# Kernel tuning notes

Measured on AMD Instinct MI355X. Metric: run time of the kernel, lower is better.

The kernel has to match this reference:

```python
import jax, jax.numpy as jnp
import numpy as np
from jax import lax

B = 16384  # batch; original torch module runs unbatched (1,5,27), we vectorize over B


def _conv(x, w, b, ph):
    # NCHW conv with kernel (kh,1), padding (ph,0), stride 1
    y = lax.conv_general_dilated(x, w, (1, 1), [(ph, ph), (0, 0)],
                                 dimension_numbers=('NCHW', 'OIHW', 'NCHW'))
    return y + b[None, :, None, None]


def _sl(x, w, b):
    # Semi_Linear: shared Linear applied over every (channel, height) slice ->
    # algebraically a single batched matmul on the last axis. w: (out,in)
    return jnp.einsum('bchw,ow->bcho', x, w) + b


def setup_inputs() -> dict:
    key = jax.random.key(0)
    ks = iter(jax.random.split(key, 40))
    def p(shape):
        return jax.random.normal(next(ks), shape, jnp.float32) * 0.05
    d = dict(
        x=jax.random.normal(next(ks), (B, 1, 5, 27), jnp.float32),
        w0a=p((5, 1, 3, 1)), b0a=p((5,)),
        wl0=p((18, 27)), bl0=p((18,)),
        w0b=p((25, 5, 3, 1)), b0b=p((25,)),
        w0c=p((25, 1, 1, 1)), b0c=p((25,)),
        wr0=p((18, 27)), br0=p((18,)),
        w1=p((75, 25, 2, 1)), b1=p((75,)),
        wl1=p((10, 18)), bl1=p((10,)),
        w2=p((125, 75, 2, 1)), b2=p((125,)),
        wa=p((125, 25, 3, 1)), ba=p((125,)),
        wra=p((10, 18)), bra=p((10,)),
        w0=p((300, 125, 2, 1)), b0=p((300,)),
        wl2=p((5, 10)), bl2=p((5,)),
        w0b2=p((512, 300, 2, 1)), b0b2=p((512,)),
        w0c2=p((512, 125, 3, 1)), b0c2=p((512,)),
        wr02=p((5, 10)), br02=p((5,)),
    )
    return d


def reference(x, w0a, b0a, wl0, bl0, w0b, b0b, w0c, b0c, wr0, br0,
              w1, b1, wl1, bl1, w2, b2, wa, ba, wra, bra,
              w0, b0, wl2, bl2, w0b2, b0b2, w0c2, b0c2, wr02, br02):
    # stage 0
    z = _conv(x, w0a, b0a, 1)                      # (B,5,5,27)
    z = jax.nn.relu(_sl(z, wl0, bl0))              # (B,5,5,18)
    z = _conv(z, w0b, b0b, 1)                      # (B,25,5,18)
    y = _conv(_sl(x, wr0, br0), w0c, b0c, 0)       # (B,25,5,18)
    x1 = z + y
    # stage 1
    z = _conv(x1, w1, b1, 0)                       # (B,75,4,18)
    z = jax.nn.relu(_sl(z, wl1, bl1))              # (B,75,4,10)
    z = _conv(z, w2, b2, 0)                        # (B,125,3,10)
    y = _conv(_sl(x1, wra, bra), wa, ba, 0)        # (B,125,3,10)
    x2 = z + y
    # stage 2
    z = _conv(x2, w0, b0, 0)                       # (B,300,2,10)
    z = jax.nn.relu(_sl(z, wl2, bl2))              # (B,300,2,5)
    z = _conv(z, w0b2, b0b2, 0)                    # (B,512,1,5)
    y = _conv(_sl(x2, wr02, br02), w0c2, b0c2, 0)  # (B,512,1,5)
    return z + y
```

## Files before the change

### kernel.cpp

```cpp
#include <hip/hip_runtime.h>
#include <stdint.h>


#define WB2T_OFF 0
#define WC2T_OFF 307200
#define W0T_OFF  499200
#define W1T_OFF  574200
#define WAT_OFF  577950
#define W2T_OFF  587325
#define SUM0_OFF 606075
#define SUM1_OFF 606093
#define SUM2_OFF 606103
#define WT_TOTAL 606108

__global__ __launch_bounds__(256)
void transpose_w(const float* __restrict__ w1, const float* __restrict__ wa,
                 const float* __restrict__ w2, const float* __restrict__ w0,
                 const float* __restrict__ wb2, const float* __restrict__ wc2,
                 const float* __restrict__ wl0, const float* __restrict__ wl1,
                 const float* __restrict__ wl2,
                 float* __restrict__ ws) {
  int i = blockIdx.x * 256 + threadIdx.x;
  if (i < 3750) {
    int co = i / 50, k = i % 50;
    ws[W1T_OFF + k*75 + co] = w1[i];
  } else if (i < 13125) {
    int j = i - 3750; int co = j / 75, k = j % 75;
    ws[WAT_OFF + k*125 + co] = wa[j];
  } else if (i < 31875) {
    int j = i - 13125; int co = j / 150, k = j % 150;
    ws[W2T_OFF + k*125 + co] = w2[j];
  } else if (i < 106875) {
    int j = i - 31875; int co = j / 250, k = j % 250;
    ws[W0T_OFF + k*300 + co] = w0[j];
  } else if (i < 414075) {
    int j = i - 106875; int co = j / 600, k = j % 600;
    ws[WB2T_OFF + k*512 + co] = wb2[j];
  } else if (i < 606075) {
    int j = i - 414075; int co = j / 375, k = j % 375;
    ws[WC2T_OFF + k*512 + co] = wc2[j];
  } else if (i < 606093) {
    int j = i - 606075; float s = 0.f;
    for (int w = 0; w < 27; ++w) s += wl0[j*27 + w];
    ws[SUM0_OFF + j] = s;
  } else if (i < 606103) {
    int j = i - 606093; float s = 0.f;
    for (int w = 0; w < 18; ++w) s += wl1[j*18 + w];
    ws[SUM1_OFF + j] = s;
  } else if (i < 606108) {
    int j = i - 606103; float s = 0.f;
    for (int w = 0; w < 10; ++w) s += wl2[j*10 + w];
    ws[SUM2_OFF + j] = s;
  }
}

template<int N>
__device__ __forceinline__ void ldrow(float* r, const float* p) {
  #pragma unroll
  for (int i = 0; i < N/4; ++i) {
    float4 q = reinterpret_cast<const float4*>(p)[i];
    r[4*i+0] = q.x; r[4*i+1] = q.y; r[4*i+2] = q.z; r[4*i+3] = q.w;
  }
}
template<int N>
__device__ __forceinline__ void strow(float* p, const float* r) {
  #pragma unroll
  for (int i = 0; i < N/4; ++i) {
    float4 q; q.x = r[4*i+0]; q.y = r[4*i+1]; q.z = r[4*i+2]; q.w = r[4*i+3];
    reinterpret_cast<float4*>(p)[i] = q;
  }
}

#define POOL   10112
#define X1_O   0
#define SX_O   2500
#define XS0_O  2640
#define T90_O  2740
#define Z0SL_O 2840
#define X1S_O  2500
#define Z1S_O  4500
#define T2_O   8100
#define X2_O   0
#define T3_O   8100
#define X2S_O  4500
#define Z2S_O  0

__global__ __launch_bounds__(256, 2)
void fused_net(const float* __restrict__ xg,
  const float* __restrict__ w0a_, const float* __restrict__ b0a_,
  const float* __restrict__ wl0_, const float* __restrict__ bl0_,
  const float* __restrict__ w0b_, const float* __restrict__ b0b_,
  const float* __restrict__ w0c_, const float* __restrict__ b0c_,
  const float* __restrict__ wr0_, const float* __restrict__ br0_,
  const float* __restrict__ b1_,
  const float* __restrict__ wl1_, const float* __restrict__ bl1_,
  const float* __restrict__ b2_,
  const float* __restrict__ ba_,
  const float* __restrict__ wra_, const float* __restrict__ bra_,
  const float* __restrict__ b0_,
  const float* __restrict__ wl2_, const float* __restrict__ bl2_,
  const float* __restrict__ b0b2_,
  const float* __restrict__ b0c2_,
  const float* __restrict__ wr02_,const float* __restrict__ br02_,
  const float* __restrict__ w1t, const float* __restrict__ wat,
  const float* __restrict__ w2t, const float* __restrict__ w0t,
  const float* __restrict__ wb2t, const float* __restrict__ wc2t,
  const float* __restrict__ sums,
  float* __restrict__ outg, int Btot)
{
  __shared__ __align__(16) float S[2*POOL];
  const int tid = threadIdx.x;
  const int b0 = blockIdx.x * 2;

  for (int i = tid; i < 270; i += 256) {
    int samp = i / 135, j = i % 135;
    int h = j / 27, w = j % 27;
    float v = 0.f;
    if (b0 + samp < Btot) v = xg[(size_t)(b0 + samp) * 135 + j];
    S[samp*POOL + SX_O + h*28 + w] = v;
  }
  __syncthreads();

  if (tid < 30) {
    int samp = tid / 15, r = tid % 15, h = r / 3, o0 = (r % 3) * 6;
    float* P = S + samp*POOL;
    float row[28]; ldrow<28>(row, P + SX_O + h*28);
    float xs[6], t9[6];
    #pragma unroll
    for (int k = 0; k < 6; ++k) { xs[k] = 0.f; t9[k] = br0_[o0 + k]; }
    for (int w = 0; w < 27; ++w) {
      float rv = row[w];
      #pragma unroll
      for (int k = 0; k < 6; ++k) {
        xs[k] += rv * wl0_[(o0 + k)*27 + w];
        t9[k] += rv * wr0_[(o0 + k)*27 + w];
      }
    }
    #pragma unroll
    for (int k = 0; k < 6; ++k) {
      P[XS0_O + h*20 + o0 + k] = xs[k];
      P[T90_O + h*20 + o0 + k] = t9[k];
    }
  }
  __syncthreads();

  if (tid < 50) {
    int samp = tid / 25, r = tid % 25, co = r / 5, h = r % 5;
    float* P = S + samp*POOL;
    float acc[20];
    float bc = b0a_[co];
    #pragma unroll
    for (int o = 0; o < 18; ++o) acc[o] = bc * sums[o] + bl0_[o];
    acc[18] = 0.f; acc[19] = 0.f;
    #pragma unroll
    for (int dh = 0; dh < 3; ++dh) {
      int hi = h + dh - 1;
      if (hi >= 0 && hi < 5) {
        float wf = w0a_[co*3 + dh];
        float row[20]; ldrow<20>(row, P + XS0_O + hi*20);
        #pragma unroll
        for (int o = 0; o < 18; ++o) acc[o] += row[o] * wf;
      }
    }
    #pragma unroll
    for (int o = 0; o < 18; ++o) acc[o] = fmaxf(acc[o], 0.f);
    strow<20>(P + Z0SL_O + (co*5 + h)*20, acc);
  }
  __syncthreads();

  if (tid < 250) {
    int samp = tid / 125, r = tid % 125, h = r / 25, co = r % 25;
    float* P = S + samp*POOL;
    float tr[20]; ldrow<20>(tr, P + T90_O + h*20);
    float wc = w0c_[co];
    float base = b0b_[co] + b0c_[co];
    float acc[20];
    #pragma unroll
    for (int o = 0; o < 18; ++o) acc[o] = base + tr[o]*wc;
    acc[18] = 0.f; acc[19] = 0.f;
    #pragma unroll
    for (int dh = 0; dh < 3; ++dh) {
      int hi = h + dh - 1;
      if (hi >= 0 && hi < 5) {
        #pragma unroll
        for (int ci = 0; ci < 5; ++ci) {
          float wgt = w0b_[(co*5 + ci)*3 + dh];
          float row[20]; ldrow<20>(row, P + Z0SL_O + (ci*5 + hi)*20);
          #pragma unroll
          for (int o = 0; o < 18; ++o) acc[o] += row[o] * wgt;
        }
      }
    }
    strow<20>(P + X1_O + (co*5 + h)*20, acc);
  }
  __syncthreads();

  if (tid < 250) {
    int samp = tid / 125, r = tid % 125, h = r / 25, c = r % 25;
    float* P = S + samp*POOL;
    float row[20]; ldrow<20>(row, P + X1_O + (c*5 + h)*20);
    float t2[12], x1s[12];
    #pragma unroll
    for (int o = 0; o < 10; ++o) {
      float a = bra_[o], s = 0.f;
      #pragma unroll
      for (int w = 0; w < 18; ++w) {
        a += row[w] * wra_[o*18 + w];
        s += row[w] * wl1_[o*18 + w];
      }
      t2[o] = a; x1s[o] = s;
    }
    t2[10] = t2[11] = 0.f; x1s[10] = x1s[11] = 0.f;
    strow<12>(P + T2_O  + (c*5 + h)*12, t2);
    strow<12>(P + X1S_O + (c*5 + h)*12, x1s);
  }
  __syncthreads();

  for (int t = tid; t < 300; t += 256) {
    int samp = t / 150, r = t % 150, co = r >> 1, h0 = (r & 1) * 2;
    float* P = S + samp*POOL;
    float acc[2][10];
    float bc = b1_[co];
    #pragma unroll
    for (int o = 0; o < 10; ++o) {
      float b = bc * sums[18 + o] + bl1_[o];
      acc[0][o] = b; acc[1][o] = b;
    }
    for (int ci = 0; ci < 25; ++ci) {
      float wx = w1t[(ci*2 + 0)*75 + co];
      float wy = w1t[(ci*2 + 1)*75 + co];
      float r0[12], r1[12], r2[12];
      ldrow<12>(r0, P + X1S_O + (ci*5 + h0    )*12);
      ldrow<12>(r1, P + X1S_O + (ci*5 + h0 + 1)*12);
      ldrow<12>(r2, P + X1S_O + (ci*5 + h0 + 2)*12);
      #pragma unroll
      for (int o = 0; o < 10; ++o) {
        acc[0][o] += r0[o]*wx + r1[o]*wy;
        acc[1][o] += r1[o]*wx + r2[o]*wy;
      }
    }
    #pragma unroll
    for (int hh = 0; hh < 2; ++hh) {
      float out[12];
      #pragma unroll
      for (int o = 0; o < 10; ++o) out[o] = fmaxf(acc[hh][o], 0.f);
      out[10] = 0.f; out[11] = 0.f;
      strow<12>(P + Z1S_O + (co*4 + h0 + hh)*12, out);
    }
  }
  __syncthreads();

  if (tid < 250) {
    int samp = tid / 125, co = tid % 125;
    float* P = S + samp*POOL;
    float acc[3][10];
    float bias = b2_[co] + ba_[co];
    #pragma unroll
    for (int h = 0; h < 3; ++h)
      #pragma unroll
      for (int w = 0; w < 10; ++w) acc[h][w] = bias;
    for (int ci = 0; ci < 25; ++ci) {
      float wf0 = wat[(ci*3 + 0)*125 + co];
      float wf1 = wat[(ci*3 + 1)*125 + co];
      float wf2 = wat[(ci*3 + 2)*125 + co];
      float rr[5][12];
      #pragma unroll
      for (int hh = 0; hh < 5; ++hh) ldrow<12>(rr[hh], P + T2_O + (ci*5 + hh)*12);
      #pragma unroll
      for (int h = 0; h < 3; ++h)
        #pragma unroll
        for (int w = 0; w < 10; ++w)
          acc[h][w] += rr[h][w]*wf0 + rr[h+1][w]*wf1 + rr[h+2][w]*wf2;
    }
    for (int ci = 0; ci < 75; ++ci) {
      float wx = w2t[(ci*2 + 0)*125 + co];
      float wy = w2t[(ci*2 + 1)*125 + co];
      float rr[4][12];
      #pragma unroll
      for (int hh = 0; hh < 4; ++hh) ldrow<12>(rr[hh], P + Z1S_O + (ci*4 + hh)*12);
      #pragma unroll
      for (int h = 0; h < 3; ++h)
        #pragma unroll
        for (int w = 0; w < 10; ++w)
          acc[h][w] += rr[h][w]*wx + rr[h+1][w]*wy;
    }
    #pragma unroll
    for (int h = 0; h < 3; ++h) {
      float out[12];
      #pragma unroll
      for (int w = 0; w < 10; ++w) out[w] = acc[h][w];
      out[10] = 0.f; out[11] = 0.f;
      strow<12>(P + X2_O + (co*3 + h)*12, out);
    }
  }
  __syncthreads();

  if (tid < 250) {
    int samp = tid / 125, c = tid % 125;
    float* P = S + samp*POOL;
    float rr[3][12];
    #pragma unroll
    for (int h = 0; h < 3; ++h) ldrow<12>(rr[h], P + X2_O + (c*3 + h)*12);
    float t3[16];
    #pragma unroll
    for (int h = 0; h < 3; ++h) {
      float x2s[8];
      #pragma unroll
      for (int o = 0; o < 5; ++o) {
        float a = br02_[o], s = 0.f;
        #pragma unroll
        for (int w = 0; w < 10; ++w) {
          a += rr[h][w] * wr02_[o*10 + w];
          s += rr[h][w] * wl2_[o*10 + w];
        }
        t3[h*5 + o] = a; x2s[o] = s;
      }
      x2s[5] = x2s[6] = x2s[7] = 0.f;
      strow<8>(P + X2S_O + (c*3 + h)*8, x2s);
    }
    t3[15] = 0.f;
    strow<16>(P + T3_O + c*16, t3);
  }
  __syncthreads();

  for (int t = tid; t < 300; t += 256) {
    int samp = t / 150, q2 = t % 150, co = q2 * 2;
    float* P = S + samp*POOL;
    float acc[2][2][5];
    #pragma unroll
    for (int j = 0; j < 2; ++j) {
      float bc = b0_[co + j];
      #pragma unroll
      for (int o = 0; o < 5; ++o) {
        float b = bc * sums[28 + o] + bl2_[o];
        acc[j][0][o] = b; acc[j][1][o] = b;
      }
    }
    for (int ci = 0; ci < 125; ++ci) {
      float2 wxv = *reinterpret_cast<const float2*>(w0t + (ci*2 + 0)*300 + co);
      float2 wyv = *reinterpret_cast<const float2*>(w0t + (ci*2 + 1)*300 + co);
      float a0[8], a1[8], a2[8];
      ldrow<8>(a0, P + X2S_O + (ci*3 + 0)*8);
      ldrow<8>(a1, P + X2S_O + (ci*3 + 1)*8);
      ldrow<8>(a2, P + X2S_O + (ci*3 + 2)*8);
      float wx[2] = {wxv.x, wxv.y};
      float wy[2] = {wyv.x, wyv.y};
      #pragma unroll
      for (int j = 0; j < 2; ++j)
        #pragma unroll
        for (int o = 0; o < 5; ++o) {
          acc[j][0][o] += a0[o]*wx[j] + a1[o]*wy[j];
          acc[j][1][o] += a1[o]*wx[j] + a2[o]*wy[j];
        }
    }
    #pragma unroll
    for (int j = 0; j < 2; ++j) {
      float out[12];
      #pragma unroll
      for (int h = 0; h < 2; ++h)
        #pragma unroll
        for (int o = 0; o < 5; ++o) out[h*5 + o] = fmaxf(acc[j][h][o], 0.f);
      out[10] = 0.f; out[11] = 0.f;
      strow<12>(P + Z2S_O + (co + j)*12, out);
    }
  }
  __syncthreads();

  {
    int samp = tid >> 7, coq = tid & 127;
    int co = coq * 4;
    float* P = S + samp*POOL;
    float acc[4][5];
    #pragma unroll
    for (int j = 0; j < 4; ++j) {
      float bb = b0b2_[co + j] + b0c2_[co + j];
      #pragma unroll
      for (int w = 0; w < 5; ++w) acc[j][w] = bb;
    }
    for (int ci = 0; ci < 300; ++ci) {
      float a[12]; ldrow<12>(a, P + Z2S_O + ci*12);
      float4 uxv = *reinterpret_cast<const float4*>(wb2t + (ci*2 + 0)*512 + co);
      float4 uyv = *reinterpret_cast<const float4*>(wb2t + (ci*2 + 1)*512 + co);
      float ux[4] = {uxv.x, uxv.y, uxv.z, uxv.w};
      float uy[4] = {uyv.x, uyv.y, uyv.z, uyv.w};
      #pragma unroll
      for (int j = 0; j < 4; ++j)
        #pragma unroll
        for (int w = 0; w < 5; ++w)
          acc[j][w] += a[w]*ux[j] + a[5 + w]*uy[j];
    }
    for (int ci = 0; ci < 125; ++ci) {
      float t3[16]; ldrow<16>(t3, P + T3_O + ci*16);
      float4 u0v = *reinterpret_cast<const float4*>(wc2t + (ci*3 + 0)*512 + co);
      float4 u1v = *reinterpret_cast<const float4*>(wc2t + (ci*3 + 1)*512 + co);
      float4 u2v = *reinterpret_cast<const float4*>(wc2t + (ci*3 + 2)*512 + co);
      float u0[4] = {u0v.x, u0v.y, u0v.z, u0v.w};
      float u1[4] = {u1v.x, u1v.y, u1v.z, u1v.w};
      float u2[4] = {u2v.x, u2v.y, u2v.z, u2v.w};
      #pragma unroll
      for (int j = 0; j < 4; ++j)
        #pragma unroll
        for (int w = 0; w < 5; ++w)
          acc[j][w] += t3[w]*u0[j] + t3[5 + w]*u1[j] + t3[10 + w]*u2[j];
    }
    if (b0 + samp < Btot) {
      float* ob = outg + (size_t)(b0 + samp) * 2560 + co*5;
      float flat[20];
      #pragma unroll
      for (int j = 0; j < 4; ++j)
        #pragma unroll
        for (int w = 0; w < 5; ++w) flat[j*5 + w] = acc[j][w];
      strow<20>(ob, flat);
    }
  }
}

extern "C" void kernel_launch(void* const* d_in, const int* in_sizes, int n_in,
                              void* d_out, int out_size, void* d_ws, size_t ws_size,
                              hipStream_t stream) {
  (void)in_sizes; (void)n_in; (void)ws_size;
  const float* p[31];
  for (int i = 0; i < 31; ++i) p[i] = (const float*)d_in[i];
  float* ws = (float*)d_ws;

  transpose_w<<<(WT_TOTAL + 255) / 256, 256, 0, stream>>>(
      p[11] , p[17] , p[15] , p[21] ,
      p[25] , p[27] ,
      p[3] , p[13] , p[23] , ws);

  int Btot = out_size / 2560;
  if (Btot <= 0) return;
  int nb = (Btot + 1) >> 1;
  fused_net<<<nb, 256, 0, stream>>>(
      p[0],
      p[1],  p[2],  p[3],  p[4],  p[5],  p[6],  p[7],  p[8],  p[9],  p[10],
      p[12],
      p[13], p[14],
      p[16],
      p[18],
      p[19], p[20],
      p[22],
      p[23], p[24],
      p[26],
      p[28],
      p[29], p[30],
      ws + W1T_OFF, ws + WAT_OFF, ws + W2T_OFF, ws + W0T_OFF,
      ws + WB2T_OFF, ws + WC2T_OFF,
      ws + SUM0_OFF,
      (float*)d_out, Btot);
}
```

Before: 3.075 ms.

## Concentrate late stages on two wavefronts with more output channels per thread

The stage-1 second conv, stage-2 first conv and final 512-channel conv now run on only 128 of the 256 threads, one wavefront per sample. Each thread computes 2, 5 or 8 output channels instead of 1, 2 or 4. A block-parity rotation picks which half of the block is active, so odd and even blocks use different SIMD slots. The goal is more register-level reuse of shared-memory activation rows and wider weight loads per FMA. The cost is half the threads sitting idle in these stages, higher register pressure, and possible occupancy loss.

After: 4.020 ms. 30.7% more time.

```diff
diff --git a/kernel.cpp b/kernel.cpp
--- a/kernel.cpp
+++ b/kernel.cpp
@@ -111,6 +111,7 @@
   __shared__ __align__(16) float S[2*POOL];
   const int tid = threadIdx.x;
   const int b0 = blockIdx.x * 2;
+  const int rot = ((int)(blockIdx.x & 1)) << 7;
 
   for (int i = tid; i < 270; i += 256) {
     int samp = i / 135, j = i % 135;
@@ -250,47 +251,75 @@
   }
   __syncthreads();
 
-  if (tid < 250) {
-    int samp = tid / 125, co = tid % 125;
-    float* P = S + samp*POOL;
-    float acc[3][10];
-    float bias = b2_[co] + ba_[co];
-    #pragma unroll
-    for (int h = 0; h < 3; ++h)
-      #pragma unroll
-      for (int w = 0; w < 10; ++w) acc[h][w] = bias;
-    for (int ci = 0; ci < 25; ++ci) {
-      float wf0 = wat[(ci*3 + 0)*125 + co];
-      float wf1 = wat[(ci*3 + 1)*125 + co];
-      float wf2 = wat[(ci*3 + 2)*125 + co];
-      float rr[5][12];
-      #pragma unroll
-      for (int hh = 0; hh < 5; ++hh) ldrow<12>(rr[hh], P + T2_O + (ci*5 + hh)*12);
-      #pragma unroll
-      for (int h = 0; h < 3; ++h)
-        #pragma unroll
-        for (int w = 0; w < 10; ++w)
-          acc[h][w] += rr[h][w]*wf0 + rr[h+1][w]*wf1 + rr[h+2][w]*wf2;
-    }
-    for (int ci = 0; ci < 75; ++ci) {
-      float wx = w2t[(ci*2 + 0)*125 + co];
-      float wy = w2t[(ci*2 + 1)*125 + co];
-      float rr[4][12];
-      #pragma unroll
-      for (int hh = 0; hh < 4; ++hh) ldrow<12>(rr[hh], P + Z1S_O + (ci*4 + hh)*12);
-      #pragma unroll
-      for (int h = 0; h < 3; ++h)
-        #pragma unroll
-        for (int w = 0; w < 10; ++w)
-          acc[h][w] += rr[h][w]*wx + rr[h+1][w]*wy;
-    }
-    #pragma unroll
-    for (int h = 0; h < 3; ++h) {
-      float out[12];
-      #pragma unroll
-      for (int w = 0; w < 10; ++w) out[w] = acc[h][w];
-      out[10] = 0.f; out[11] = 0.f;
-      strow<12>(P + X2_O + (co*3 + h)*12, out);
+  {
+    int at = tid - rot;
+    if (at >= 0 && at < 128) {
+      int samp = at >> 6, lane = at & 63;
+      if (lane < 63) {
+        int co0 = lane * 2;
+        int two = (co0 + 1 < 125);
+        int co1 = two ? co0 + 1 : co0;
+        float* P = S + samp*POOL;
+        float acc[2][3][10];
+        float bi0 = b2_[co0] + ba_[co0];
+        float bi1 = b2_[co1] + ba_[co1];
+        #pragma unroll
+        for (int h = 0; h < 3; ++h)
+          #pragma unroll
+          for (int w = 0; w < 10; ++w) { acc[0][h][w] = bi0; acc[1][h][w] = bi1; }
+        for (int ci = 0; ci < 25; ++ci) {
+          float wf[2][3];
+          #pragma unroll
+          for (int d = 0; d < 3; ++d) {
+            wf[0][d] = wat[(ci*3 + d)*125 + co0];
+            wf[1][d] = wat[(ci*3 + d)*125 + co1];
+          }
+          float rr[5][12];
+          #pragma unroll
+          for (int hh = 0; hh < 5; ++hh) ldrow<12>(rr[hh], P + T2_O + (ci*5 + hh)*12);
+          #pragma unroll
+          for (int j = 0; j < 2; ++j)
+            #pragma unroll
+            for (int h = 0; h < 3; ++h)
+              #pragma unroll
+              for (int w = 0; w < 10; ++w)
+                acc[j][h][w] += rr[h][w]*wf[j][0] + rr[h+1][w]*wf[j][1] + rr[h+2][w]*wf[j][2];
+        }
+        for (int ci = 0; ci < 75; ++ci) {
+          float wx0 = w2t[(ci*2 + 0)*125 + co0];
+          float wx1 = w2t[(ci*2 + 0)*125 + co1];
+          float wy0 = w2t[(ci*2 + 1)*125 + co0];
+          float wy1 = w2t[(ci*2 + 1)*125 + co1];
+          float rr[4][12];
+          #pragma unroll
+          for (int hh = 0; hh < 4; ++hh) ldrow<12>(rr[hh], P + Z1S_O + (ci*4 + hh)*12);
+          #pragma unroll
+          for (int h = 0; h < 3; ++h)
+            #pragma unroll
+            for (int w = 0; w < 10; ++w) {
+              acc[0][h][w] += rr[h][w]*wx0 + rr[h+1][w]*wy0;
+              acc[1][h][w] += rr[h][w]*wx1 + rr[h+1][w]*wy1;
+            }
+        }
+        #pragma unroll
+        for (int h = 0; h < 3; ++h) {
+          float out[12];
+          #pragma unroll
+          for (int w = 0; w < 10; ++w) out[w] = acc[0][h][w];
+          out[10] = 0.f; out[11] = 0.f;
+          strow<12>(P + X2_O + (co0*3 + h)*12, out);
+        }
+        if (two) {
+          #pragma unroll
+          for (int h = 0; h < 3; ++h) {
+            float out[12];
+            #pragma unroll
+            for (int w = 0; w < 10; ++w) out[w] = acc[1][h][w];
+            out[10] = 0.f; out[11] = 0.f;
+            strow<12>(P + X2_O + (co1*3 + h)*12, out);
+          }
+        }
+      }
     }
   }
   __syncthreads();
@@ -323,94 +352,102 @@
   }
   __syncthreads();
 
-  for (int t = tid; t < 300; t += 256) {
-    int samp = t / 150, q2 = t % 150, co = q2 * 2;
-    float* P = S + samp*POOL;
-    float acc[2][2][5];
-    #pragma unroll
-    for (int j = 0; j < 2; ++j) {
-      float bc = b0_[co + j];
-      #pragma unroll
-      for (int o = 0; o < 5; ++o) {
-        float b = bc * sums[28 + o] + bl2_[o];
-        acc[j][0][o] = b; acc[j][1][o] = b;
-      }
-    }
-    for (int ci = 0; ci < 125; ++ci) {
-      float2 wxv = *reinterpret_cast<const float2*>(w0t + (ci*2 + 0)*300 + co);
-      float2 wyv = *reinterpret_cast<const float2*>(w0t + (ci*2 + 1)*300 + co);
-      float a0[8], a1[8], a2[8];
-      ldrow<8>(a0, P + X2S_O + (ci*3 + 0)*8);
-      ldrow<8>(a1, P + X2S_O + (ci*3 + 1)*8);
-      ldrow<8>(a2, P + X2S_O + (ci*3 + 2)*8);
-      float wx[2] = {wxv.x, wxv.y};
-      float wy[2] = {wyv.x, wyv.y};
-      #pragma unroll
-      for (int j = 0; j < 2; ++j)
-        #pragma unroll
-        for (int o = 0; o < 5; ++o) {
-          acc[j][0][o] += a0[o]*wx[j] + a1[o]*wy[j];
-          acc[j][1][o] += a1[o]*wx[j] + a2[o]*wy[j];
-        }
-    }
-    #pragma unroll
-    for (int j = 0; j < 2; ++j) {
-      float out[12];
-      #pragma unroll
-      for (int h = 0; h < 2; ++h)
-        #pragma unroll
-        for (int o = 0; o < 5; ++o) out[h*5 + o] = fmaxf(acc[j][h][o], 0.f);
-      out[10] = 0.f; out[11] = 0.f;
-      strow<12>(P + Z2S_O + (co + j)*12, out);
-    }
-  }
-  __syncthreads();
-
   {
-    int samp = tid >> 7, coq = tid & 127;
-    int co = coq * 4;
-    float* P = S + samp*POOL;
-    float acc[4][5];
-    #pragma unroll
-    for (int j = 0; j < 4; ++j) {
-      float bb = b0b2_[co + j] + b0c2_[co + j];
-      #pragma unroll
-      for (int w = 0; w < 5; ++w) acc[j][w] = bb;
-    }
-    for (int ci = 0; ci < 300; ++ci) {
-      float a[12]; ldrow<12>(a, P + Z2S_O + ci*12);
-      float4 uxv = *reinterpret_cast<const float4*>(wb2t + (ci*2 + 0)*512 + co);
-      float4 uyv = *reinterpret_cast<const float4*>(wb2t + (ci*2 + 1)*512 + co);
-      float ux[4] = {uxv.x, uxv.y, uxv.z, uxv.w};
-      float uy[4] = {uyv.x, uyv.y, uyv.z, uyv.w};
-      #pragma unroll
-      for (int j = 0; j < 4; ++j)
-        #pragma unroll
-        for (int w = 0; w < 5; ++w)
-          acc[j][w] += a[w]*ux[j] + a[5 + w]*uy[j];
-    }
-    for (int ci = 0; ci < 125; ++ci) {
-      float t3[16]; ldrow<16>(t3, P + T3_O + ci*16);
-      float4 u0v = *reinterpret_cast<const float4*>(wc2t + (ci*3 + 0)*512 + co);
-      float4 u1v = *reinterpret_cast<const float4*>(wc2t + (ci*3 + 1)*512 + co);
-      float4 u2v = *reinterpret_cast<const float4*>(wc2t + (ci*3 + 2)*512 + co);
-      float u0[4] = {u0v.x, u0v.y, u0v.z, u0v.w};
-      float u1[4] = {u1v.x, u1v.y, u1v.z, u1v.w};
-      float u2[4] = {u2v.x, u2v.y, u2v.z, u2v.w};
-      #pragma unroll
-      for (int j = 0; j < 4; ++j)
-        #pragma unroll
-        for (int w = 0; w < 5; ++w)
-          acc[j][w] += t3[w]*u0[j] + t3[5 + w]*u1[j] + t3[10 + w]*u2[j];
-    }
-    if (b0 + samp < Btot) {
-      float* ob = outg + (size_t)(b0 + samp) * 2560 + co*5;
-      float flat[20];
-      #pragma unroll
-      for (int j = 0; j < 4; ++j)
-        #pragma unroll
-        for (int w = 0; w < 5; ++w) flat[j*5 + w] = acc[j][w];
-      strow<20>(ob, flat);
+    int at = tid - rot;
+    if (at >= 0 && at < 128) {
+      int samp = at >> 6, lane = at & 63;
+      if (lane < 60) {
+        int co = lane * 5;
+        float* P = S + samp*POOL;
+        float acc[5][2][5];
+        #pragma unroll
+        for (int j = 0; j < 5; ++j) {
+          float bc = b0_[co + j];
+          #pragma unroll
+          for (int o = 0; o < 5; ++o) {
+            float b = bc * sums[28 + o] + bl2_[o];
+            acc[j][0][o] = b; acc[j][1][o] = b;
+          }
+        }
+        for (int ci = 0; ci < 125; ++ci) {
+          float wx[5], wy[5];
+          #pragma unroll
+          for (int j = 0; j < 5; ++j) {
+            wx[j] = w0t[(ci*2 + 0)*300 + co + j];
+            wy[j] = w0t[(ci*2 + 1)*300 + co + j];
+          }
+          float a0[8], a1[8], a2[8];
+          ldrow<8>(a0, P + X2S_O + (ci*3 + 0)*8);
+          ldrow<8>(a1, P + X2S_O + (ci*3 + 1)*8);
+          ldrow<8>(a2, P + X2S_O + (ci*3 + 2)*8);
+          #pragma unroll
+          for (int j = 0; j < 5; ++j)
+            #pragma unroll
+            for (int o = 0; o < 5; ++o) {
+              acc[j][0][o] += a0[o]*wx[j] + a1[o]*wy[j];
+              acc[j][1][o] += a1[o]*wx[j] + a2[o]*wy[j];
+            }
+        }
+        #pragma unroll
+        for (int j = 0; j < 5; ++j) {
+          float out[12];
+          #pragma unroll
+          for (int h = 0; h < 2; ++h)
+            #pragma unroll
+            for (int o = 0; o < 5; ++o) out[h*5 + o] = fmaxf(acc[j][h][o], 0.f);
+          out[10] = 0.f; out[11] = 0.f;
+          strow<12>(P + Z2S_O + (co + j)*12, out);
+        }
+      }
+    }
+  }
+  __syncthreads();
+
+  {
+    int at = tid - rot;
+    if (at >= 0 && at < 128) {
+      int samp = at >> 6, lane = at & 63;
+      int co = lane * 8;
+      float* P = S + samp*POOL;
+      float acc[8][5];
+      #pragma unroll
+      for (int j = 0; j < 8; ++j) {
+        float bb = b0b2_[co + j] + b0c2_[co + j];
+        #pragma unroll
+        for (int w = 0; w < 5; ++w) acc[j][w] = bb;
+      }
+      for (int ci = 0; ci < 300; ++ci) {
+        float a[12]; ldrow<12>(a, P + Z2S_O + ci*12);
+        float ux[8], uy[8];
+        ldrow<8>(ux, wb2t + (ci*2 + 0)*512 + co);
+        ldrow<8>(uy, wb2t + (ci*2 + 1)*512 + co);
+        #pragma unroll
+        for (int j = 0; j < 8; ++j)
+          #pragma unroll
+          for (int w = 0; w < 5; ++w)
+            acc[j][w] += a[w]*ux[j] + a[5 + w]*uy[j];
+      }
+      for (int ci = 0; ci < 125; ++ci) {
+        float t3[16]; ldrow<16>(t3, P + T3_O + ci*16);
+        float u0[8], u1[8], u2[8];
+        ldrow<8>(u0, wc2t + (ci*3 + 0)*512 + co);
+        ldrow<8>(u1, wc2t + (ci*3 + 1)*512 + co);
+        ldrow<8>(u2, wc2t + (ci*3 + 2)*512 + co);
+        #pragma unroll
+        for (int j = 0; j < 8; ++j)
+          #pragma unroll
+          for (int w = 0; w < 5; ++w)
+            acc[j][w] += t3[w]*u0[j] + t3[5 + w]*u1[j] + t3[10 + w]*u2[j];
+      }
+      if (b0 + samp < Btot) {
+        float* ob = outg + (size_t)(b0 + samp) * 2560 + co*5;
+        float flat[40];
+        #pragma unroll
+        for (int j = 0; j < 8; ++j)
+          #pragma unroll
+          for (int w = 0; w < 5; ++w) flat[j*5 + w] = acc[j][w];
+        strow<40>(ob, flat);
+      }
     }
   }
 }
```

## Move later-stage intermediates to global scratch and use persistent grid-stride blocks

Applied to the files above, without the earlier changes.

Shrinks shared memory per block to the stage-0 buffers and moves stage 1 and stage 2 intermediates into per-block global workspace scratch. The kernel becomes persistent: at most 1024 blocks (fewer if workspace is small) loop over sample pairs. The aim is higher occupancy from less LDS per block, at the cost of routing the heavy later-stage reads through global memory and cache instead of LDS. There is also a risk of too few blocks if the workspace is small.

Result: slower. 5.905 ms (+92.0%).

```diff
diff --git a/kernel.cpp b/kernel.cpp
--- a/kernel.cpp
+++ b/kernel.cpp
@@ -71,19 +71,21 @@
   }
 }
 
-#define POOL   10112
-#define X1_O   0
+#define LPOOL  3340
+#define X1L_O  0
 #define SX_O   2500
 #define XS0_O  2640
 #define T90_O  2740
 #define Z0SL_O 2840
+
+#define GPOOL  10112
+#define X2_O   0
+#define Z2S_O  0
 #define X1S_O  2500
 #define Z1S_O  4500
+#define X2S_O  4500
 #define T2_O   8100
-#define X2_O   0
 #define T3_O   8100
-#define X2S_O  4500
-#define Z2S_O  0
 
 __global__ __launch_bounds__(256, 2)
 void fused_net(const float* __restrict__ xg,
@@ -106,319 +108,326 @@
   const float* __restrict__ w2t, const float* __restrict__ w0t,
   const float* __restrict__ wb2t, const float* __restrict__ wc2t,
   const float* __restrict__ sums,
-  float* __restrict__ outg, int Btot)
+  float* scr,
+  float* __restrict__ outg, int Btot, int npairs, int NB)
 {
-  __shared__ __align__(16) float S[2*POOL];
+  __shared__ __align__(16) float S[2*LPOOL];
   const int tid = threadIdx.x;
-  const int b0 = blockIdx.x * 2;
-
-  for (int i = tid; i < 270; i += 256) {
-    int samp = i / 135, j = i % 135;
-    int h = j / 27, w = j % 27;
-    float v = 0.f;
-    if (b0 + samp < Btot) v = xg[(size_t)(b0 + samp) * 135 + j];
-    S[samp*POOL + SX_O + h*28 + w] = v;
-  }
-  __syncthreads();
-
-  if (tid < 30) {
-    int samp = tid / 15, r = tid % 15, h = r / 3, o0 = (r % 3) * 6;
-    float* P = S + samp*POOL;
-    float row[28]; ldrow<28>(row, P + SX_O + h*28);
-    float xs[6], t9[6];
-    #pragma unroll
-    for (int k = 0; k < 6; ++k) { xs[k] = 0.f; t9[k] = br0_[o0 + k]; }
-    for (int w = 0; w < 27; ++w) {
-      float rv = row[w];
+  float* G = scr + (size_t)blockIdx.x * (2*GPOOL);
+
+  for (int p = blockIdx.x; p < npairs; p += NB) {
+    const int b0 = p * 2;
+
+    for (int i = tid; i < 270; i += 256) {
+      int samp = i / 135, j = i % 135;
+      int h = j / 27, w = j % 27;
+      float v = 0.f;
+      if (b0 + samp < Btot) v = xg[(size_t)(b0 + samp) * 135 + j];
+      S[samp*LPOOL + SX_O + h*28 + w] = v;
+    }
+    __syncthreads();
+
+    if (tid < 30) {
+      int samp = tid / 15, r = tid % 15, h = r / 3, o0 = (r % 3) * 6;
+      float* L = S + samp*LPOOL;
+      float row[28]; ldrow<28>(row, L + SX_O + h*28);
+      float xs[6], t9[6];
+      #pragma unroll
+      for (int k = 0; k < 6; ++k) { xs[k] = 0.f; t9[k] = br0_[o0 + k]; }
+      for (int w = 0; w < 27; ++w) {
+        float rv = row[w];
+        #pragma unroll
+        for (int k = 0; k < 6; ++k) {
+          xs[k] += rv * wl0_[(o0 + k)*27 + w];
+          t9[k] += rv * wr0_[(o0 + k)*27 + w];
+        }
+      }
       #pragma unroll
       for (int k = 0; k < 6; ++k) {
-        xs[k] += rv * wl0_[(o0 + k)*27 + w];
-        t9[k] += rv * wr0_[(o0 + k)*27 + w];
-      }
-    }
-    #pragma unroll
-    for (int k = 0; k < 6; ++k) {
-      P[XS0_O + h*20 + o0 + k] = xs[k];
-      P[T90_O + h*20 + o0 + k] = t9[k];
-    }
-  }
-  __syncthreads();
-
-  if (tid < 50) {
-    int samp = tid / 25, r = tid % 25, co = r / 5, h = r % 5;
-    float* P = S + samp*POOL;
-    float acc[20];
-    float bc = b0a_[co];
-    #pragma unroll
-    for (int o = 0; o < 18; ++o) acc[o] = bc * sums[o] + bl0_[o];
-    acc[18] = 0.f; acc[19] = 0.f;
-    #pragma unroll
-    for (int dh = 0; dh < 3; ++dh) {
-      int hi = h + dh - 1;
-      if (hi >= 0 && hi < 5) {
-        float wf = w0a_[co*3 + dh];
-        float row[20]; ldrow<20>(row, P + XS0_O + hi*20);
-        #pragma unroll
-        for (int o = 0; o < 18; ++o) acc[o] += row[o] * wf;
-      }
-    }
-    #pragma unroll
-    for (int o = 0; o < 18; ++o) acc[o] = fmaxf(acc[o], 0.f);
-    strow<20>(P + Z0SL_O + (co*5 + h)*20, acc);
-  }
-  __syncthreads();
-
-  if (tid < 250) {
-    int samp = tid / 125, r = tid % 125, h = r / 25, co = r % 25;
-    float* P = S + samp*POOL;
-    float tr[20]; ldrow<20>(tr, P + T90_O + h*20);
-    float wc = w0c_[co];
-    float base = b0b_[co] + b0c_[co];
-    float acc[20];
-    #pragma unroll
-    for (int o = 0; o < 18; ++o) acc[o] = base + tr[o]*wc;
-    acc[18] = 0.f; acc[19] = 0.f;
-    #pragma unroll
-    for (int dh = 0; dh < 3; ++dh) {
-      int hi = h + dh - 1;
-      if (hi >= 0 && hi < 5) {
-        #pragma unroll
-        for (int ci = 0; ci < 5; ++ci) {
-          float wgt = w0b_[(co*5 + ci)*3 + dh];
-          float row[20]; ldrow<20>(row, P + Z0SL_O + (ci*5 + hi)*20);
-          #pragma unroll
-          for (int o = 0; o < 18; ++o) acc[o] += row[o] * wgt;
-        }
-      }
-    }
-    strow<20>(P + X1_O + (co*5 + h)*20, acc);
-  }
-  __syncthreads();
-
-  if (tid < 250) {
-    int samp = tid / 125, r = tid % 125, h = r / 25, c = r % 25;
-    float* P = S + samp*POOL;
-    float row[20]; ldrow<20>(row, P + X1_O + (c*5 + h)*20);
-    float t2[12], x1s[12];
-    #pragma unroll
-    for (int o = 0; o < 10; ++o) {
-      float a = bra_[o], s = 0.f;
-      #pragma unroll
-      for (int w = 0; w < 18; ++w) {
-        a += row[w] * wra_[o*18 + w];
-        s += row[w] * wl1_[o*18 + w];
-      }
-      t2[o] = a; x1s[o] = s;
-    }
-    t2[10] = t2[11] = 0.f; x1s[10] = x1s[11] = 0.f;
-    strow<12>(P + T2_O  + (c*5 + h)*12, t2);
-    strow<12>(P + X1S_O + (c*5 + h)*12, x1s);
-  }
-  __syncthreads();
-
-  for (int t = tid; t < 300; t += 256) {
-    int samp = t / 150, r = t % 150, co = r >> 1, h0 = (r & 1) * 2;
-    float* P = S + samp*POOL;
-    float acc[2][10];
-    float bc = b1_[co];
-    #pragma unroll
-    for (int o = 0; o < 10; ++o) {
-      float b = bc * sums[18 + o] + bl1_[o];
-      acc[0][o] = b; acc[1][o] = b;
-    }
-    for (int ci = 0; ci < 25; ++ci) {
-      float wx = w1t[(ci*2 + 0)*75 + co];
-      float wy = w1t[(ci*2 + 1)*75 + co];
-      float r0[12], r1[12], r2[12];
-      ldrow<12>(r0, P + X1S_O + (ci*5 + h0    )*12);
-      ldrow<12>(r1, P + X1S_O + (ci*5 + h0 + 1)*12);
-      ldrow<12>(r2, P + X1S_O + (ci*5 + h0 + 2)*12);
+        L[XS0_O + h*20 + o0 + k] = xs[k];
+        L[T90_O + h*20 + o0 + k] = t9[k];
+      }
+    }
+    __syncthreads();
+
+    if (tid < 50) {
+      int samp = tid / 25, r = tid % 25, co = r / 5, h = r % 5;
+      float* L = S + samp*LPOOL;
+      float acc[20];
+      float bc = b0a_[co];
+      #pragma unroll
+      for (int o = 0; o < 18; ++o) acc[o] = bc * sums[o] + bl0_[o];
+      acc[18] = 0.f; acc[19] = 0.f;
+      #pragma unroll
+      for (int dh = 0; dh < 3; ++dh) {
+        int hi = h + dh - 1;
+        if (hi >= 0 && hi < 5) {
+          float wf = w0a_[co*3 + dh];
+          float row[20]; ldrow<20>(row, L + XS0_O + hi*20);
+          #pragma unroll
+          for (int o = 0; o < 18; ++o) acc[o] += row[o] * wf;
+        }
+      }
+      #pragma unroll
+      for (int o = 0; o < 18; ++o) acc[o] = fmaxf(acc[o], 0.f);
+      strow<20>(L + Z0SL_O + (co*5 + h)*20, acc);
+    }
+    __syncthreads();
+
+    if (tid < 250) {
+      int samp = tid / 125, r = tid % 125, h = r / 25, co = r % 25;
+      float* L = S + samp*LPOOL;
+      float tr[20]; ldrow<20>(tr, L + T90_O + h*20);
+      float wc = w0c_[co];
+      float base = b0b_[co] + b0c_[co];
+      float acc[20];
+      #pragma unroll
+      for (int o = 0; o < 18; ++o) acc[o] = base + tr[o]*wc;
+      acc[18] = 0.f; acc[19] = 0.f;
+      #pragma unroll
+      for (int dh = 0; dh < 3; ++dh) {
+        int hi = h + dh - 1;
+        if (hi >= 0 && hi < 5) {
+          #pragma unroll
+          for (int ci = 0; ci < 5; ++ci) {
+            float wgt = w0b_[(co*5 + ci)*3 + dh];
+            float row[20]; ldrow<20>(row, L + Z0SL_O + (ci*5 + hi)*20);
+            #pragma unroll
+            for (int o = 0; o < 18; ++o) acc[o] += row[o] * wgt;
+          }
+        }
+      }
+      strow<20>(L + X1L_O + (co*5 + h)*20, acc);
+    }
+    __syncthreads();
+
+    if (tid < 250) {
+      int samp = tid / 125, r = tid % 125, h = r / 25, c = r % 25;
+      float* L = S + samp*LPOOL;
+      float* Gp = G + samp*GPOOL;
+      float row[20]; ldrow<20>(row, L + X1L_O + (c*5 + h)*20);
+      float t2[12], x1s[12];
       #pragma unroll
       for (int o = 0; o < 10; ++o) {
-        acc[0][o] += r0[o]*wx + r1[o]*wy;
-        acc[1][o] += r1[o]*wx + r2[o]*wy;
-      }
-    }
-    #pragma unroll
-    for (int hh = 0; hh < 2; ++hh) {
-      float out[12];
-      #pragma unroll
-      for (int o = 0; o < 10; ++o) out[o] = fmaxf(acc[hh][o], 0.f);
-      out[10] = 0.f; out[11] = 0.f;
-      strow<12>(P + Z1S_O + (co*4 + h0 + hh)*12, out);
-    }
-  }
-  __syncthreads();
-
-  if (tid < 250) {
-    int samp = tid / 125, co = tid % 125;
-    float* P = S + samp*POOL;
-    float acc[3][10];
-    float bias = b2_[co] + ba_[co];
-    #pragma unroll
-    for (int h = 0; h < 3; ++h)
-      #pragma unroll
-      for (int w = 0; w < 10; ++w) acc[h][w] = bias;
-    for (int ci = 0; ci < 25; ++ci) {
-      float wf0 = wat[(ci*3 + 0)*125 + co];
-      float wf1 = wat[(ci*3 + 1)*125 + co];
-      float wf2 = wat[(ci*3 + 2)*125 + co];
-      float rr[5][12];
-      #pragma unroll
-      for (int hh = 0; hh < 5; ++hh) ldrow<12>(rr[hh], P + T2_O + (ci*5 + hh)*12);
+        float a = bra_[o], s = 0.f;
+        #pragma unroll
+        for (int w = 0; w < 18; ++w) {
+          a += row[w] * wra_[o*18 + w];
+          s += row[w] * wl1_[o*18 + w];
+        }
+        t2[o] = a; x1s[o] = s;
+      }
+      t2[10] = t2[11] = 0.f; x1s[10] = x1s[11] = 0.f;
+      strow<12>(Gp + T2_O  + (c*5 + h)*12, t2);
+      strow<12>(Gp + X1S_O + (c*5 + h)*12, x1s);
+    }
+    __syncthreads();
+
+    for (int t = tid; t < 300; t += 256) {
+      int samp = t / 150, r = t % 150, co = r >> 1, h0 = (r & 1) * 2;
+      float* Gp = G + samp*GPOOL;
+      float acc[2][10];
+      float bc = b1_[co];
+      #pragma unroll
+      for (int o = 0; o < 10; ++o) {
+        float b = bc * sums[18 + o] + bl1_[o];
+        acc[0][o] = b; acc[1][o] = b;
+      }
+      for (int ci = 0; ci < 25; ++ci) {
+        float wx = w1t[(ci*2 + 0)*75 + co];
+        float wy = w1t[(ci*2 + 1)*75 + co];
+        float r0[12], r1[12], r2[12];
+        ldrow<12>(r0, Gp + X1S_O + (ci*5 + h0    )*12);
+        ldrow<12>(r1, Gp + X1S_O + (ci*5 + h0 + 1)*12);
+        ldrow<12>(r2, Gp + X1S_O + (ci*5 + h0 + 2)*12);
+        #pragma unroll
+        for (int o = 0; o < 10; ++o) {
+          acc[0][o] += r0[o]*wx + r1[o]*wy;
+          acc[1][o] += r1[o]*wx + r2[o]*wy;
+        }
+      }
+      #pragma unroll
+      for (int hh = 0; hh < 2; ++hh) {
+        float out[12];
+        #pragma unroll
+        for (int o = 0; o < 10; ++o) out[o] = fmaxf(acc[hh][o], 0.f);
+        out[10] = 0.f; out[11] = 0.f;
+        strow<12>(Gp + Z1S_O + (co*4 + h0 + hh)*12, out);
+      }
+    }
+    __syncthreads();
+
+    if (tid < 250) {
+      int samp = tid / 125, co = tid % 125;
+      float* Gp = G + samp*GPOOL;
+      float acc[3][10];
+      float bias = b2_[co] + ba_[co];
       #pragma unroll
       for (int h = 0; h < 3; ++h)
         #pragma unroll
-        for (int w = 0; w < 10; ++w)
-          acc[h][w] += rr[h][w]*wf0 + rr[h+1][w]*wf1 + rr[h+2][w]*wf2;
-    }
-    for (int ci = 0; ci < 75; ++ci) {
-      float wx = w2t[(ci*2 + 0)*125 + co];
-      float wy = w2t[(ci*2 + 1)*125 + co];
-      float rr[4][12];
-      #pragma unroll
-      for (int hh = 0; hh < 4; ++hh) ldrow<12>(rr[hh], P + Z1S_O + (ci*4 + hh)*12);
-      #pragma unroll
-      for (int h = 0; h < 3; ++h)
-        #pragma unroll
-        for (int w = 0; w < 10; ++w)
-          acc[h][w] += rr[h][w]*wx + rr[h+1][w]*wy;
-    }
-    #pragma unroll
-    for (int h = 0; h < 3; ++h) {
-      float out[12];
-      #pragma unroll
-      for (int w = 0; w < 10; ++w) out[w] = acc[h][w];
-      out[10] = 0.f; out[11] = 0.f;
-      strow<12>(P + X2_O + (co*3 + h)*12, out);
-    }
-  }
-  __syncthreads();
-
-  if (tid < 250) {
-    int samp = tid / 125, c = tid % 125;
-    float* P = S + samp*POOL;
-    float rr[3][12];
-    #pragma unroll
-    for (int h = 0; h < 3; ++h) ldrow<12>(rr[h], P + X2_O + (c*3 + h)*12);
-    float t3[16];
-    #pragma unroll
-    for (int h = 0; h < 3; ++h) {
-      float x2s[8];
-      #pragma unroll
-      for (int o = 0; o < 5; ++o) {
-        float a = br02_[o], s = 0.f;
-        #pragma unroll
-        for (int w = 0; w < 10; ++w) {
-          a += rr[h][w] * wr02_[o*10 + w];
-          s += rr[h][w] * wl2_[o*10 + w];
-        }
-        t3[h*5 + o] = a; x2s[o] = s;
-      }
-      x2s[5] = x2s[6] = x2s[7] = 0.f;
-      strow<8>(P + X2S_O + (c*3 + h)*8, x2s);
-    }
-    t3[15] = 0.f;
-    strow<16>(P + T3_O + c*16, t3);
-  }
-  __syncthreads();
-
-  for (int t = tid; t < 300; t += 256) {
-    int samp = t / 150, q2 = t % 150, co = q2 * 2;
-    float* P = S + samp*POOL;
-    float acc[2][2][5];
-    #pragma unroll
-    for (int j = 0; j < 2; ++j) {
-      float bc = b0_[co + j];
-      #pragma unroll
-      for (int o = 0; o < 5; ++o) {
-        float b = bc * sums[28 + o] + bl2_[o];
-        acc[j][0][o] = b; acc[j][1][o] = b;
-      }
-    }
-    for (int ci = 0; ci < 125; ++ci) {
-      float2 wxv = *reinterpret_cast<const float2*>(w0t + (ci*2 + 0)*300 + co);
-      float2 wyv = *reinterpret_cast<const float2*>(w0t + (ci*2 + 1)*300 + co);
-      float a0[8], a1[8], a2[8];
-      ldrow<8>(a0, P + X2S_O + (ci*3 + 0)*8);
-      ldrow<8>(a1, P + X2S_O + (ci*3 + 1)*8);
-      ldrow<8>(a2, P + X2S_O + (ci*3 + 2)*8);
-      float wx[2] = {wxv.x, wxv.y};
-      float wy[2] = {wyv.x, wyv.y};
-      #pragma unroll
-      for (int j = 0; j < 2; ++j)
+        for (int w = 0; w < 10; ++w) acc[h][w] = bias;
+      for (int ci = 0; ci < 25; ++ci) {
+        float wf0 = wat[(ci*3 + 0)*125 + co];
+        float wf1 = wat[(ci*3 + 1)*125 + co];
+        float wf2 = wat[(ci*3 + 2)*125 + co];
+        float rr[5][12];
+        #pragma unroll
+        for (int hh = 0; hh < 5; ++hh) ldrow<12>(rr[hh], Gp + T2_O + (ci*5 + hh)*12);
+        #pragma unroll
+        for (int h = 0; h < 3; ++h)
+          #pragma unroll
+          for (int w = 0; w < 10; ++w)
+            acc[h][w] += rr[h][w]*wf0 + rr[h+1][w]*wf1 + rr[h+2][w]*wf2;
+      }
+      for (int ci = 0; ci < 75; ++ci) {
+        float wx = w2t[(ci*2 + 0)*125 + co];
+        float wy = w2t[(ci*2 + 1)*125 + co];
+        float rr[4][12];
+        #pragma unroll
+        for (int hh = 0; hh < 4; ++hh) ldrow<12>(rr[hh], Gp + Z1S_O + (ci*4 + hh)*12);
+        #pragma unroll
+        for (int h = 0; h < 3; ++h)
+          #pragma unroll
+          for (int w = 0; w < 10; ++w)
+            acc[h][w] += rr[h][w]*wx + rr[h+1][w]*wy;
+      }
+      #pragma unroll
+      for (int h = 0; h < 3; ++h) {
+        float out[12];
+        #pragma unroll
+        for (int w = 0; w < 10; ++w) out[w] = acc[h][w];
+        out[10] = 0.f; out[11] = 0.f;
+        strow<12>(Gp + X2_O + (co*3 + h)*12, out);
+      }
+    }
+    __syncthreads();
+
+    if (tid < 250) {
+      int samp = tid / 125, c = tid % 125;
+      float* Gp = G + samp*GPOOL;
+      float rr[3][12];
+      #pragma unroll
+      for (int h = 0; h < 3; ++h) ldrow<12>(rr[h], Gp + X2_O + (c*3 + h)*12);
+      float t3[16];
+      #pragma unroll
+      for (int h = 0; h < 3; ++h) {
+        float x2s[8];
         #pragma unroll
         for (int o = 0; o < 5; ++o) {
-          acc[j][0][o] += a0[o]*wx[j] + a1[o]*wy[j];
-          acc[j][1][o] += a1[o]*wx[j] + a2[o]*wy[j];
-        }
-    }
-    #pragma unroll
-    for (int j = 0; j < 2; ++j) {
-      float out[12];
-      #pragma unroll
-      for (int h = 0; h < 2; ++h)
-        #pragma unroll
-        for (int o = 0; o < 5; ++o) out[h*5 + o] = fmaxf(acc[j][h][o], 0.f);
-      out[10] = 0.f; out[11] = 0.f;
-      strow<12>(P + Z2S_O + (co + j)*12, out);
-    }
-  }
-  __syncthreads();
-
-  {
-    int samp = tid >> 7, coq = tid & 127;
-    int co = coq * 4;
-    float* P = S + samp*POOL;
-    float acc[4][5];
-    #pragma unroll
-    for (int j = 0; j < 4; ++j) {
-      float bb = b0b2_[co + j] + b0c2_[co + j];
-      #pragma unroll
-      for (int w = 0; w < 5; ++w) acc[j][w] = bb;
-    }
-    for (int ci = 0; ci < 300; ++ci) {
-      float a[12]; ldrow<12>(a, P + Z2S_O + ci*12);
-      float4 uxv = *reinterpret_cast<const float4*>(wb2t + (ci*2 + 0)*512 + co);
-      float4 uyv = *reinterpret_cast<const float4*>(wb2t + (ci*2 + 1)*512 + co);
-      float ux[4] = {uxv.x, uxv.y, uxv.z, uxv.w};
-      float uy[4] = {uyv.x, uyv.y, uyv.z, uyv.w};
-      #pragma unroll
-      for (int j = 0; j < 4; ++j)
-        #pragma unroll
-        for (int w = 0; w < 5; ++w)
-          acc[j][w] += a[w]*ux[j] + a[5 + w]*uy[j];
-    }
-    for (int ci = 0; ci < 125; ++ci) {
-      float t3[16]; ldrow<16>(t3, P + T3_O + ci*16);
-      float4 u0v = *reinterpret_cast<const float4*>(wc2t + (ci*3 + 0)*512 + co);
-      float4 u1v = *reinterpret_cast<const float4*>(wc2t + (ci*3 + 1)*512 + co);
-      float4 u2v = *reinterpret_cast<const float4*>(wc2t + (ci*3 + 2)*512 + co);
-      float u0[4] = {u0v.x, u0v.y, u0v.z, u0v.w};
-      float u1[4] = {u1v.x, u1v.y, u1v.z, u1v.w};
-      float u2[4] = {u2v.x, u2v.y, u2v.z, u2v.w};
-      #pragma unroll
-      for (int j = 0; j < 4; ++j)
-        #pragma unroll
-        for (int w = 0; w < 5; ++w)
-          acc[j][w] += t3[w]*u0[j] + t3[5 + w]*u1[j] + t3[10 + w]*u2[j];
-    }
-    if (b0 + samp < Btot) {
-      float* ob = outg + (size_t)(b0 + samp) * 2560 + co*5;
-      float flat[20];
-      #pragma unroll
-      for (int j = 0; j < 4; ++j)
-        #pragma unroll
-        for (int w = 0; w < 5; ++w) flat[j*5 + w] = acc[j][w];
-      strow<20>(ob, flat);
-    }
+          float a = br02_[o], s = 0.f;
+          #pragma unroll
+          for (int w = 0; w < 10; ++w) {
+            a += rr[h][w] * wr02_[o*10 + w];
+            s += rr[h][w] * wl2_[o*10 + w];
+          }
+          t3[h*5 + o] = a; x2s[o] = s;
+        }
+        x2s[5] = x2s[6] = x2s[7] = 0.f;
+        strow<8>(Gp + X2S_O + (c*3 + h)*8, x2s);
+      }
+      t3[15] = 0.f;
+      strow<16>(Gp + T3_O + c*16, t3);
+    }
+    __syncthreads();
+
+    for (int t = tid; t < 300; t += 256) {
+      int samp = t / 150, q2 = t % 150, co = q2 * 2;
+      float* Gp = G + samp*GPOOL;
+      float acc[2][2][5];
+      #pragma unroll
+      for (int j = 0; j < 2; ++j) {
+        float bc = b0_[co + j];
+        #pragma unroll
+        for (int o = 0; o < 5; ++o) {
+          float b = bc * sums[28 + o] + bl2_[o];
+          acc[j][0][o] = b; acc[j][1][o] = b;
+        }
+      }
+      for (int ci = 0; ci < 125; ++ci) {
+        float2 wxv = *reinterpret_cast<const float2*>(w0t + (ci*2 + 0)*300 + co);
+        float2 wyv = *reinterpret_cast<const float2*>(w0t + (ci*2 + 1)*300 + co);
+        float a0[8], a1[8], a2[8];
+        ldrow<8>(a0, Gp + X2S_O + (ci*3 + 0)*8);
+        ldrow<8>(a1, Gp + X2S_O + (ci*3 + 1)*8);
+        ldrow<8>(a2, Gp + X2S_O + (ci*3 + 2)*8);
+        float wx[2] = {wxv.x, wxv.y};
+        float wy[2] = {wyv.x, wyv.y};
+        #pragma unroll
+        for (int j = 0; j < 2; ++j)
+          #pragma unroll
+          for (int o = 0; o < 5; ++o) {
+            acc[j][0][o] += a0[o]*wx[j] + a1[o]*wy[j];
+            acc[j][1][o] += a1[o]*wx[j] + a2[o]*wy[j];
+          }
+      }
+      #pragma unroll
+      for (int j = 0; j < 2; ++j) {
+        float out[12];
+        #pragma unroll
+        for (int h = 0; h < 2; ++h)
+          #pragma unroll
+          for (int o = 0; o < 5; ++o) out[h*5 + o] = fmaxf(acc[j][h][o], 0.f);
+        out[10] = 0.f; out[11] = 0.f;
+        strow<12>(Gp + Z2S_O + (co + j)*12, out);
+      }
+    }
+    __syncthreads();
+
+    {
+      int samp = tid >> 7, coq = tid & 127;
+      int co = coq * 4;
+      float* Gp = G + samp*GPOOL;
+      float acc[4][5];
+      #pragma unroll
+      for (int j = 0; j < 4; ++j) {
+        float bb = b0b2_[co + j] + b0c2_[co + j];
+        #pragma unroll
+        for (int w = 0; w < 5; ++w) acc[j][w] = bb;
+      }
+      for (int ci = 0; ci < 300; ++ci) {
+        float a[12]; ldrow<12>(a, Gp + Z2S_O + ci*12);
+        float4 uxv = *reinterpret_cast<const float4*>(wb2t + (ci*2 + 0)*512 + co);
+        float4 uyv = *reinterpret_cast<const float4*>(wb2t + (ci*2 + 1)*512 + co);
+        float ux[4] = {uxv.x, uxv.y, uxv.z, uxv.w};
+        float uy[4] = {uyv.x, uyv.y, uyv.z, uyv.w};
+        #pragma unroll
+        for (int j = 0; j < 4; ++j)
+          #pragma unroll
+          for (int w = 0; w < 5; ++w)
+            acc[j][w] += a[w]*ux[j] + a[5 + w]*uy[j];
+      }
+      for (int ci = 0; ci < 125; ++ci) {
+        float t3[16]; ldrow<16>(t3, Gp + T3_O + ci*16);
+        float4 u0v = *reinterpret_cast<const float4*>(wc2t + (ci*3 + 0)*512 + co);
+        float4 u1v = *reinterpret_cast<const float4*>(wc2t + (ci*3 + 1)*512 + co);
+        float4 u2v = *reinterpret_cast<const float4*>(wc2t + (ci*3 + 2)*512 + co);
+        float u0[4] = {u0v.x, u0v.y, u0v.z, u0v.w};
+        float u1[4] = {u1v.x, u1v.y, u1v.z, u1v.w};
+        float u2[4] = {u2v.x, u2v.y, u2v.z, u2v.w};
+        #pragma unroll
+        for (int j = 0; j < 4; ++j)
+          #pragma unroll
+          for (int w = 0; w < 5; ++w)
+            acc[j][w] += t3[w]*u0[j] + t3[5 + w]*u1[j] + t3[10 + w]*u2[j];
+      }
+      if (b0 + samp < Btot) {
+        float* ob = outg + (size_t)(b0 + samp) * 2560 + co*5;
+        float flat[20];
+        #pragma unroll
+        for (int j = 0; j < 4; ++j)
+          #pragma unroll
+          for (int w = 0; w < 5; ++w) flat[j*5 + w] = acc[j][w];
+        strow<20>(ob, flat);
+      }
+    }
+    __syncthreads();
   }
 }
 
 extern "C" void kernel_launch(void* const* d_in, const int* in_sizes, int n_in,
                               void* d_out, int out_size, void* d_ws, size_t ws_size,
                               hipStream_t stream) {
-  (void)in_sizes; (void)n_in; (void)ws_size;
+  (void)in_sizes; (void)n_in;
   const float* p[31];
   for (int i = 0; i < 31; ++i) p[i] = (const float*)d_in[i];
   float* ws = (float*)d_ws;
@@ -430,8 +439,15 @@
 
   int Btot = out_size / 2560;
   if (Btot <= 0) return;
-  int nb = (Btot + 1) >> 1;
-  fused_net<<<nb, 256, 0, stream>>>(
+  int npairs = (Btot + 1) >> 1;
+
+  long long avail = (long long)(ws_size / 4) - WT_TOTAL;
+  long long fit = avail / (2 * GPOOL);
+  int NB = (int)(fit < 1024 ? fit : 1024);
+  if (NB > npairs) NB = npairs;
+  if (NB < 1) NB = 1;
+
+  fused_net<<<NB, 256, 0, stream>>>(
       p[0],
       p[1],  p[2],  p[3],  p[4],  p[5],  p[6],  p[7],  p[8],  p[9],  p[10],
       p[12],
@@ -447,5 +463,6 @@
       ws + W1T_OFF, ws + WAT_OFF, ws + W2T_OFF, ws + W0T_OFF,
       ws + WB2T_OFF, ws + WC2T_OFF,
       ws + SUM0_OFF,
-      (float*)d_out, Btot);
+      ws + WT_TOTAL,
+      (float*)d_out, Btot, npairs, NB);
 }
```
